# Performance work log

Hardware: AMD Instinct MI355X
Metric: run time of the kernel (lower is better)

## Reference

```python
import jax, jax.numpy as jnp
import numpy as np
import math

H = 2048          # hidden_size
NH = 16           # num_attn_heads
HD = H // NH      # attn head dim = 128
NFW = 4           # num_lact_heads
FD = H // NFW     # fw head dim = 512
DH = FD           # inter_multi = 1.0
CHUNK = 512       # lact_chunk_size
WINDOW = 2048     # window_size
ROPE_BASE = 500000.0
BASE_LR_INV = math.log(math.expm1(0.001))  # inv_softplus(1e-3)


def rmsnorm(x, w, eps=1e-6):
    return x * jax.lax.rsqrt(jnp.mean(x * x, axis=-1, keepdims=True) + eps) * w


def l2norm(x, eps=1e-12):
    return x * jax.lax.rsqrt(jnp.sum(x * x, axis=-1, keepdims=True) + eps)


def rope(x):  # x: [b, h, s, d], half-split convention
    d = x.shape[-1]
    s = x.shape[2]
    inv = 1.0 / (ROPE_BASE ** (jnp.arange(d // 2, dtype=jnp.float32) / (d // 2)))
    f = jnp.arange(s, dtype=jnp.float32)[:, None] * inv[None, :]  # [s, d/2]
    cos, sin = jnp.cos(f), jnp.sin(f)
    x1, x2 = x[..., : d // 2], x[..., d // 2:]
    return jnp.concatenate([x1 * cos - x2 * sin, x2 * cos + x1 * sin], axis=-1)


def setup_inputs() -> dict:
    key = jax.random.key(0)
    ks = jax.random.split(key, 8)
    b, s = 2, 2048
    return {
        "hidden_states": jax.random.normal(ks[0], (b, s, H), jnp.float32),
        "qkv_w": jax.random.normal(ks[1], (3 * H, H), jnp.float32) / math.sqrt(H),
        "q_norm_w": jnp.ones((H,), jnp.float32),
        "k_norm_w": jnp.ones((H,), jnp.float32),
        "qk_scale": jnp.ones((H, 2), jnp.float32),
        "qk_offset": jnp.zeros((H, 2), jnp.float32),
        "lr_w": jax.random.normal(ks[2], (3 * NFW, H), jnp.float32) / math.sqrt(H),
        "lr_b": jnp.zeros((3 * NFW,), jnp.float32),
        "w0": jax.random.normal(ks[3], (NFW, DH, FD), jnp.float32) / math.sqrt(FD),
        "w1": jax.random.normal(ks[4], (NFW, FD, DH), jnp.float32) / math.sqrt(DH),
        "w2": jax.random.normal(ks[5], (NFW, DH, FD), jnp.float32) / math.sqrt(FD),
        "ttt_norm_w": jnp.ones((FD,), jnp.float32),
        "o_proj_w": jax.random.normal(ks[6], (H, H), jnp.float32) / math.sqrt(H),
    }


def reference(hidden_states, qkv_w, q_norm_w, k_norm_w, qk_scale, qk_offset,
              lr_w, lr_b, w0, w1, w2, ttt_norm_w, o_proj_w):
    x = hidden_states
    b, s, _ = x.shape
    nc = s // CHUNK

    qkv = x @ qkv_w.T
    q, k, v = jnp.split(qkv, 3, axis=-1)
    q = rmsnorm(q, q_norm_w)
    k = rmsnorm(k, k_norm_w)

    # ---- TTT (fast-weight SwiGLU) branch ----
    fq = jax.nn.silu(q * qk_scale[:, 0] + qk_offset[:, 0])
    fk = jax.nn.silu(k * qk_scale[:, 1] + qk_offset[:, 1])
    fv = jax.nn.silu(v)
    tohead = lambda t: t.reshape(b, s, NFW, FD).transpose(0, 2, 1, 3)  # [b,h,s,d]
    fq, fk, fv = l2norm(tohead(fq)), l2norm(tohead(fk)), tohead(fv)

    lr = jax.nn.softplus(x @ lr_w.T + lr_b + BASE_LR_INV)          # [b,s,3*NFW]
    lr = lr.reshape(b, s, 3, NFW).transpose(2, 0, 3, 1)[..., None]  # [3,b,h,s,1]
    lr0, lr1, lr2 = lr[0], lr[1], lr[2]

    chunkify = lambda t: t.reshape(b, NFW, nc, CHUNK, -1).transpose(2, 0, 1, 3, 4)
    qs, ks_, vs = chunkify(fq), chunkify(fk), chunkify(fv)
    l0s, l1s, l2s = chunkify(lr0), chunkify(lr1), chunkify(lr2)

    w0b = jnp.broadcast_to(w0, (b,) + w0.shape)
    w1b = jnp.broadcast_to(w1, (b,) + w1.shape)
    w2b = jnp.broadcast_to(w2, (b,) + w2.shape)

    def step(carry, xs):
        w0c, w1c, w2c = carry
        qc, kc, vc, l0, l1, l2 = xs
        # apply current fast weights to queries (strictly causal across chunks)
        hq = jax.nn.silu(jnp.einsum('bhcd,bhed->bhce', qc, w0c)) * \
             jnp.einsum('bhcd,bhed->bhce', qc, w2c)
        oc = jnp.einsum('bhce,bhde->bhcd', hq, w1c)
        # gradient-descent update on dot-product loss -sum(v * f(k))
        g1 = jnp.einsum('bhcd,bhed->bhce', kc, w0c)
        g2 = jnp.einsum('bhcd,bhed->bhce', kc, w2c)
        gate = jax.nn.silu(g1)
        hidden = gate * g2
        dhidden = jnp.einsum('bhcd,bhde->bhce', vc, w1c)  # w1^T v
        dh2 = dhidden * gate
        sig = jax.nn.sigmoid(g1)
        dh1 = dhidden * g2 * (sig * (1.0 + g1 * (1.0 - sig)))  # silu'(g1)
        w1n = w1c + jnp.einsum('bhcd,bhce->bhde', l1 * vc, hidden)
        w0n = w0c + jnp.einsum('bhce,bhcd->bhed', l0 * dh1, kc)
        w2n = w2c + jnp.einsum('bhce,bhcd->bhed', l2 * dh2, kc)
        return (w0n, w1n, w2n), oc

    _, o_chunks = jax.lax.scan(step, (w0b, w1b, w2b), (qs, ks_, vs, l0s, l1s, l2s))
    o_ttt = o_chunks.transpose(1, 2, 0, 3, 4).reshape(b, NFW, s, FD)
    o_ttt = rmsnorm(o_ttt, ttt_norm_w)
    o_ttt = o_ttt.transpose(0, 2, 1, 3).reshape(b, s, H)

    # ---- sliding-window attention branch ----
    qa = rope(q.reshape(b, s, NH, HD).transpose(0, 2, 1, 3))
    ka = rope(k.reshape(b, s, NH, HD).transpose(0, 2, 1, 3))
    va = v.reshape(b, s, NH, HD).transpose(0, 2, 1, 3)
    scores = jnp.einsum('bhqd,bhkd->bhqk', qa, ka) / math.sqrt(HD)
    i = jnp.arange(s)
    mask = (i[:, None] >= i[None, :]) & (i[:, None] - i[None, :] < WINDOW)
    scores = jnp.where(mask, scores, jnp.float32(-1e9))
    p = jax.nn.softmax(scores, axis=-1)
    attn = jnp.einsum('bhqk,bhkd->bhqd', p, va).transpose(0, 2, 1, 3).reshape(b, s, H)

    return (attn + o_ttt) @ o_proj_w.T
```

## Files before the change

kernel.cpp:

```cpp
#include <hip/hip_runtime.h>
#include <hip/hip_bf16.h>
#include <math.h>

using bf16 = __hip_bfloat16;

namespace {

constexpr int cH = 2048;
constexpr int cNH = 16;
constexpr int cHD = 128;
constexpr int cNFW = 4;
constexpr int cFD = 512;
constexpr int cS = 2048;
constexpr float cRSQRT_HD = 0.08838834764831845f;
constexpr long ZL_ = 262144;
constexpr long ZG_ = 1048576;

typedef __attribute__((ext_vector_type(8))) short short8;
typedef __attribute__((ext_vector_type(4))) float f32x4;

__device__ __forceinline__ float sigmoidf_(float x) { return 1.0f / (1.0f + __expf(-x)); }
__device__ __forceinline__ float b2f(bf16 v) { return __bfloat162float(v); }
__device__ __forceinline__ bf16 f2b(float v) { return __float2bfloat16(v); }
__device__ __forceinline__ unsigned short f2bu(float f) {
  return __builtin_bit_cast(unsigned short, __float2bfloat16(f));
}

#if defined(__has_builtin)
#if __has_builtin(__builtin_amdgcn_global_load_lds)
#define HAVE_GLOAD 1
#endif
#endif

__device__ __forceinline__ void gload16(const bf16* g, short* ldsbase) {
#ifdef HAVE_GLOAD
  __builtin_amdgcn_global_load_lds((const __attribute__((address_space(1))) void*)g,
                                   (__attribute__((address_space(3))) void*)ldsbase, 16, 0, 0);
#else
  const int l = threadIdx.x & 63;
  *(uint4*)(ldsbase + l * 8) = *(const uint4*)g;
#endif
}

__device__ __forceinline__ void stage16(const bf16* src, short* dst) {
  *(uint4*)dst = *(const uint4*)src;
  *(uint4*)(dst + 8) = *(const uint4*)(src + 8);
}

__device__ __forceinline__ void store1(float* p, float v) { *p = v; }
__device__ __forceinline__ void store1(bf16* p, float v) { *p = f2b(v); }

template <int AMODE, int BMODE>
__device__ __forceinline__ void mm_core(const bf16* __restrict__ Ab, int lda,
                                        const bf16* __restrict__ Bb, int ldb, int K,
                                        const float* __restrict__ sc,
                                        short* As, short* Bs, f32x4 acc[4][4]) {
  const int t = threadIdx.x, lane = t & 63, g = lane >> 4, c16 = lane & 15;
  const int wv = t >> 6, wm = (wv >> 1) * 64, wn = (wv & 1) * 64;
  for (int k0 = 0; k0 < K; k0 += 32) {
    __syncthreads();
    if constexpr (AMODE == 0) {
      const int ch = wv * 2;
      const bf16* g0 = Ab + (size_t)(ch * 16 + (lane >> 2)) * lda + k0 + (lane & 3) * 8;
      gload16(g0, &As[ch * 512]);
      gload16(g0 + (size_t)16 * lda, &As[ch * 512 + 512]);
    } else {
      const int kk = t >> 3, mseg = (t & 7) * 16;
      const float s = sc[k0 + kk];
      const bf16* p = Ab + (size_t)(k0 + kk) * lda + mseg;
#pragma unroll
      for (int i = 0; i < 16; ++i) As[(mseg + i) * 32 + kk] = (short)f2bu(b2f(p[i]) * s);
    }
    if constexpr (BMODE == 0) {
      const int ch = wv * 2;
      const bf16* g0 = Bb + (size_t)(ch * 16 + (lane >> 2)) * ldb + k0 + (lane & 3) * 8;
      gload16(g0, &Bs[ch * 512]);
      gload16(g0 + (size_t)16 * ldb, &Bs[ch * 512 + 512]);
    } else {
      const int kk = t >> 3, cseg = (t & 7) * 16;
      const short* p = (const short*)(Bb + (size_t)(k0 + kk) * ldb + cseg);
#pragma unroll
      for (int i = 0; i < 16; ++i) Bs[(cseg + i) * 32 + kk] = p[i];
    }
    __syncthreads();
    short8 af[4], bfr[4];
#pragma unroll
    for (int mi = 0; mi < 4; ++mi) af[mi] = *(const short8*)&As[(wm + mi * 16 + c16) * 32 + g * 8];
#pragma unroll
    for (int ni = 0; ni < 4; ++ni) bfr[ni] = *(const short8*)&Bs[(wn + ni * 16 + c16) * 32 + g * 8];
#pragma unroll
    for (int mi = 0; mi < 4; ++mi)
#pragma unroll
      for (int ni = 0; ni < 4; ++ni)
        acc[mi][ni] = __builtin_amdgcn_mfma_f32_16x16x32_bf16(af[mi], bfr[ni], acc[mi][ni], 0, 0, 0);
  }
}

template <bool ACC, bool MIR, typename TC>
__device__ __forceinline__ void mm_store(TC* Cb, bf16* Mb, int ldc, int rb, int cb, f32x4 acc[4][4]) {
  const int t = threadIdx.x, lane = t & 63, g = lane >> 4, c16 = lane & 15;
  const int wv = t >> 6, wm = (wv >> 1) * 64, wn = (wv & 1) * 64;
  const int rbase = rb + wm, cbase = cb + wn;
#pragma unroll
  for (int mi = 0; mi < 4; ++mi)
#pragma unroll
    for (int ni = 0; ni < 4; ++ni) {
      const int col = cbase + ni * 16 + c16;
#pragma unroll
      for (int r = 0; r < 4; ++r) {
        const int row = rbase + mi * 16 + g * 4 + r;
        TC* cp = Cb + (size_t)row * ldc + col;
        if constexpr (ACC) {
          float nv = *cp + acc[mi][ni][r];
          *cp = nv;
          if constexpr (MIR) Mb[(size_t)row * ldc + col] = f2b(nv);
        } else {
          store1(cp, acc[mi][ni][r]);
        }
      }
    }
}

template <typename TC, int BMODE>
__global__ __launch_bounds__(256) void k_mm(const bf16* __restrict__ A, int lda, long zsa,
                                            const bf16* __restrict__ B, int ldb, long zsb,
                                            TC* __restrict__ C, int ldc, long zsc, int K) {
  __shared__ short As[128 * 32];
  __shared__ short Bs[128 * 32];
  const int z = blockIdx.z;
  const bf16* Ab = A + (size_t)z * zsa + (size_t)blockIdx.y * 128 * lda;
  const bf16* Bb = (BMODE == 0) ? (B + (size_t)z * zsb + (size_t)blockIdx.x * 128 * ldb)
                                : (B + (size_t)z * zsb + blockIdx.x * 128);
  f32x4 acc[4][4];
  const f32x4 zero4 = {0.f, 0.f, 0.f, 0.f};
#pragma unroll
  for (int i = 0; i < 4; ++i)
#pragma unroll
    for (int j = 0; j < 4; ++j) acc[i][j] = zero4;
  mm_core<0, BMODE>(Ab, lda, Bb, ldb, K, nullptr, As, Bs, acc);
  mm_store<false, false>(C + (size_t)z * zsc, (bf16*)nullptr, ldc, blockIdx.y * 128, blockIdx.x * 128, acc);
}

__global__ __launch_bounds__(256) void k_fuse1(const bf16* __restrict__ fq, const bf16* __restrict__ fk,
                                               const bf16* __restrict__ fv,
                                               const bf16* __restrict__ w0b, const bf16* __restrict__ w1bc,
                                               const bf16* __restrict__ w2b,
                                               bf16* __restrict__ hq, bf16* __restrict__ trH,
                                               bf16* __restrict__ trD1, bf16* __restrict__ trD2,
                                               bf16* __restrict__ trK, bf16* __restrict__ trV,
                                               const float* __restrict__ lr0, const float* __restrict__ lr1,
                                               const float* __restrict__ lr2,
                                               const bf16* __restrict__ occPrev,
                                               const float* __restrict__ tw, bf16* __restrict__ y,
                                               int chunk) {
  __shared__ short S[12800];
  __shared__ float red[4];
  const int id = blockIdx.x, t = threadIdx.x;
  const size_t choff = (size_t)chunk * 262144;

  if (id < 512) {
    const int bh = id >> 6, tile = id & 63, by = tile >> 3, bx = tile & 7;
    const int lane = t & 63, g = lane >> 4, c16 = lane & 15, wv = t >> 6;
    const int wm = (wv >> 1) * 32, wn = (wv & 1) * 32;
    const bf16* Aq = fq + (size_t)bh * ZG_ + choff + (size_t)(by * 64) * cFD;
    const bf16* Ak = fk + (size_t)bh * ZG_ + choff + (size_t)(by * 64) * cFD;
    const bf16* Av = fv + (size_t)bh * ZG_ + choff + (size_t)(by * 64) * cFD;
    const bf16* B0 = w0b + (size_t)bh * ZL_ + (size_t)(bx * 64) * cFD;
    const bf16* B2 = w2b + (size_t)bh * ZL_ + (size_t)(bx * 64) * cFD;
    const bf16* B1 = w1bc + (size_t)bh * ZL_ + bx * 64;

    f32x4 acc[5][2][2];
    const f32x4 zero4 = {0.f, 0.f, 0.f, 0.f};
#pragma unroll
    for (int v = 0; v < 5; ++v)
#pragma unroll
      for (int i = 0; i < 2; ++i)
#pragma unroll
        for (int j = 0; j < 2; ++j) acc[v][i][j] = zero4;

    const int srow = wv * 16 + (lane >> 2), scol = (lane & 3) * 8;
    for (int k0 = 0; k0 < 512; k0 += 32) {
      __syncthreads();
      gload16(Aq + (size_t)srow * cFD + k0 + scol, &S[0 + wv * 512]);
      gload16(Ak + (size_t)srow * cFD + k0 + scol, &S[2048 + wv * 512]);
      gload16(Av + (size_t)srow * cFD + k0 + scol, &S[4096 + wv * 512]);
      gload16(B0 + (size_t)srow * cFD + k0 + scol, &S[6144 + wv * 512]);
      gload16(B2 + (size_t)srow * cFD + k0 + scol, &S[8192 + wv * 512]);
      {
        const int e = t & 63, kg = t >> 6;
        unsigned short u[8] __attribute__((aligned(16)));
#pragma unroll
        for (int i = 0; i < 8; ++i)
          u[i] = *(const unsigned short*)(B1 + (size_t)(k0 + kg * 8 + i) * cFD + e);
        *(uint4*)&S[10240 + e * 40 + kg * 8] = *(uint4*)u;
      }
      __syncthreads();
      short8 aq[2], ak[2], av[2], b0[2], b2[2], b1[2];
#pragma unroll
      for (int mi = 0; mi < 2; ++mi) {
        const int ro = (wm + mi * 16 + c16) * 32 + g * 8;
        aq[mi] = *(const short8*)&S[0 + ro];
        ak[mi] = *(const short8*)&S[2048 + ro];
        av[mi] = *(const short8*)&S[4096 + ro];
      }
#pragma unroll
      for (int ni = 0; ni < 2; ++ni) {
        const int ro = (wn + ni * 16 + c16) * 32 + g * 8;
        b0[ni] = *(const short8*)&S[6144 + ro];
        b2[ni] = *(const short8*)&S[8192 + ro];
        b1[ni] = *(const short8*)&S[10240 + (wn + ni * 16 + c16) * 40 + g * 8];
      }
#pragma unroll
      for (int mi = 0; mi < 2; ++mi)
#pragma unroll
        for (int ni = 0; ni < 2; ++ni) {
          acc[0][mi][ni] = __builtin_amdgcn_mfma_f32_16x16x32_bf16(aq[mi], b0[ni], acc[0][mi][ni], 0, 0, 0);
          acc[1][mi][ni] = __builtin_amdgcn_mfma_f32_16x16x32_bf16(aq[mi], b2[ni], acc[1][mi][ni], 0, 0, 0);
          acc[2][mi][ni] = __builtin_amdgcn_mfma_f32_16x16x32_bf16(ak[mi], b0[ni], acc[2][mi][ni], 0, 0, 0);
          acc[3][mi][ni] = __builtin_amdgcn_mfma_f32_16x16x32_bf16(ak[mi], b2[ni], acc[3][mi][ni], 0, 0, 0);
          acc[4][mi][ni] = __builtin_amdgcn_mfma_f32_16x16x32_bf16(av[mi], b1[ni], acc[4][mi][ni], 0, 0, 0);
        }
    }

    float l0v[2][4], l2v[2][4];
#pragma unroll
    for (int mi = 0; mi < 2; ++mi)
#pragma unroll
      for (int r = 0; r < 4; ++r) {
        const int row = by * 64 + wm + mi * 16 + g * 4 + r;
        l0v[mi][r] = lr0[bh * 2048 + chunk * 512 + row];
        l2v[mi][r] = lr2[bh * 2048 + chunk * 512 + row];
      }
#pragma unroll
    for (int mi = 0; mi < 2; ++mi)
#pragma unroll
      for (int ni = 0; ni < 2; ++ni)
#pragma unroll
        for (int r = 0; r < 4; ++r) {
          float hq1 = acc[0][mi][ni][r], hq2 = acc[1][mi][ni][r];
          float g1 = acc[2][mi][ni][r], g2 = acc[3][mi][ni][r], dh = acc[4][mi][ni][r];
          acc[0][mi][ni][r] = hq1 * sigmoidf_(hq1) * hq2;
          float sg = sigmoidf_(g1);
          float gate = g1 * sg;
          acc[1][mi][ni][r] = gate * g2;
          acc[2][mi][ni][r] = l0v[mi][r] * dh * g2 * (sg * (1.0f + g1 * (1.0f - sg)));
          acc[3][mi][ni][r] = l2v[mi][r] * dh * gate;
        }

    short* Ts = S;
    bf16* dst0 = hq + (size_t)bh * ZL_;
    bf16* dstT[3] = {trH + (size_t)bh * ZL_, trD1 + (size_t)bh * ZL_, trD2 + (size_t)bh * ZL_};
#pragma unroll
    for (int rd = 0; rd < 4; ++rd) {
      __syncthreads();
#pragma unroll
      for (int mi = 0; mi < 2; ++mi)
#pragma unroll
        for (int ni = 0; ni < 2; ++ni)
#pragma unroll
          for (int r = 0; r < 4; ++r) {
            const int row = wm + mi * 16 + g * 4 + r, col = wn + ni * 16 + c16;
            if (rd == 0) Ts[row * 66 + col] = (short)f2bu(acc[0][mi][ni][r]);
            else Ts[col * 66 + row] = (short)f2bu(acc[rd][mi][ni][r]);
          }
      __syncthreads();
      const int rr = t >> 2, cs = (t & 3) * 16;
      unsigned short u[16] __attribute__((aligned(16)));
#pragma unroll
      for (int i = 0; i < 16; ++i) u[i] = (unsigned short)Ts[rr * 66 + cs + i];
      bf16* dp = (rd == 0) ? (dst0 + (size_t)(by * 64 + rr) * cFD + bx * 64 + cs)
                           : (dstT[rd - 1] + (size_t)(bx * 64 + rr) * cFD + by * 64 + cs);
      *(uint4*)dp = *(uint4*)u;
      *(uint4*)(dp + 8) = *(uint4*)(u + 8);
    }
  } else if (id < 1536) {
    short* Ts = S;
    const int id2 = id - 512;
    const int var = id2 >> 9, bh = (id2 >> 6) & 7, by = (id2 >> 3) & 7, bx = id2 & 7;
    const bf16* src = ((var == 0) ? fk : fv) + choff + (size_t)bh * ZG_;
    bf16* dst = ((var == 0) ? trK : trV) + (size_t)bh * ZL_;
    {
      const int rr = t >> 2, cseg = (t & 3) * 16;
      if (var == 0) {
        stage16(src + (size_t)(by * 64 + rr) * cFD + bx * 64 + cseg, &Ts[rr * 72 + cseg]);
      } else {
        const float s = lr1[bh * 2048 + chunk * 512 + by * 64 + rr];
        const bf16* p = src + (size_t)(by * 64 + rr) * cFD + bx * 64 + cseg;
        unsigned short u[16] __attribute__((aligned(16)));
#pragma unroll
        for (int i = 0; i < 16; ++i) u[i] = f2bu(b2f(p[i]) * s);
        *(uint4*)&Ts[rr * 72 + cseg] = *(uint4*)u;
        *(uint4*)&Ts[rr * 72 + cseg + 8] = *(uint4*)(u + 8);
      }
    }
    __syncthreads();
    {
      const int oc_ = t >> 2, rseg = (t & 3) * 16;
      unsigned short u[16] __attribute__((aligned(16)));
#pragma unroll
      for (int i = 0; i < 16; ++i) u[i] = (unsigned short)Ts[(rseg + i) * 72 + oc_];
      bf16* dp = dst + (size_t)(bx * 64 + oc_) * cFD + by * 64 + rseg;
      *(uint4*)dp = *(uint4*)u;
      *(uint4*)(dp + 8) = *(uint4*)(u + 8);
    }
  } else {
    const int rrow = id - 1536;
    const int bh = rrow >> 9, rr = rrow & 511;
    const bf16* src = occPrev + ((size_t)bh * 512 + rr) * 512;
    float v0 = b2f(src[t]), v1 = b2f(src[t + 256]);
    float ss = v0 * v0 + v1 * v1;
    for (int d = 32; d; d >>= 1) ss += __shfl_down(ss, d);
    if ((t & 63) == 0) red[t >> 6] = ss;
    __syncthreads();
    const float rstd = rsqrtf((red[0] + red[1] + red[2] + red[3]) / cFD + 1e-6f);
    const int si = (chunk - 1) * 512 + rr;
    bf16* dst = y + ((size_t)((bh >> 2) * cS) + si) * cH + (bh & 3) * cFD;
    dst[t] = f2b(b2f(dst[t]) + v0 * rstd * tw[t]);
    dst[t + 256] = f2b(b2f(dst[t + 256]) + v1 * rstd * tw[t + 256]);
  }
}

__global__ __launch_bounds__(256) void k_updna(const bf16* __restrict__ trV, const bf16* __restrict__ trH,
                                               const bf16* __restrict__ trD1, const bf16* __restrict__ trD2,
                                               const bf16* __restrict__ trK,
                                               const bf16* __restrict__ hq, const bf16* __restrict__ w1bc,
                                               float* w0s, float* w1s, float* w2s,
                                               bf16* w0b, bf16* w1bn, bf16* w2b,
                                               bf16* __restrict__ occCur) {
  __shared__ short Sh[8192];
  const int id = blockIdx.x, t = threadIdx.x;
  if (id < 384) {
    short* As = Sh;
    short* Bs = Sh + 4096;
    const int z = id >> 4, tile = id & 15, by = tile >> 2, bx = tile & 3;
    const int var = z >> 3, bh = z & 7;
    const bf16 *Aa, *Bb;
    float* W;
    bf16* M;
    if (var == 0) {
      Aa = trV + (size_t)bh * ZL_ + (size_t)by * 128 * cFD;
      Bb = trH + (size_t)bh * ZL_ + (size_t)bx * 128 * cFD;
      W = w1s + (size_t)bh * ZL_; M = w1bn + (size_t)bh * ZL_;
    } else if (var == 1) {
      Aa = trD1 + (size_t)bh * ZL_ + (size_t)by * 128 * cFD;
      Bb = trK + (size_t)bh * ZL_ + (size_t)bx * 128 * cFD;
      W = w0s + (size_t)bh * ZL_; M = w0b + (size_t)bh * ZL_;
    } else {
      Aa = trD2 + (size_t)bh * ZL_ + (size_t)by * 128 * cFD;
      Bb = trK + (size_t)bh * ZL_ + (size_t)bx * 128 * cFD;
      W = w2s + (size_t)bh * ZL_; M = w2b + (size_t)bh * ZL_;
    }
    f32x4 acc[4][4];
    const f32x4 zero4 = {0.f, 0.f, 0.f, 0.f};
#pragma unroll
    for (int i = 0; i < 4; ++i)
#pragma unroll
      for (int j = 0; j < 4; ++j) acc[i][j] = zero4;
    mm_core<0, 0>(Aa, cFD, Bb, cFD, cFD, nullptr, As, Bs, acc);
    mm_store<true, true>(W, M, cFD, by * 128, bx * 128, acc);
  } else {
    const int id2 = id - 384;
    const int bh = id2 >> 6, tile = id2 & 63, by = tile >> 3, bx = tile & 7;
    const int lane = t & 63, g = lane >> 4, c16 = lane & 15, wv = t >> 6;
    const int wm = (wv >> 1) * 32, wn = (wv & 1) * 32;
    const bf16* Aa = hq + (size_t)bh * ZL_ + (size_t)(by * 64) * cFD;
    const bf16* Bb = w1bc + (size_t)bh * ZL_ + (size_t)(bx * 64) * cFD;
    short* As = Sh;
    short* Bs = Sh + 2048;
    f32x4 acc[2][2];
    const f32x4 zero4 = {0.f, 0.f, 0.f, 0.f};
#pragma unroll
    for (int i = 0; i < 2; ++i)
#pragma unroll
      for (int j = 0; j < 2; ++j) acc[i][j] = zero4;
    for (int k0 = 0; k0 < 512; k0 += 32) {
      __syncthreads();
      {
        const int srow = wv * 16 + (lane >> 2), scol = (lane & 3) * 8;
        gload16(Aa + (size_t)srow * cFD + k0 + scol, &As[wv * 512]);
        gload16(Bb + (size_t)srow * cFD + k0 + scol, &Bs[wv * 512]);
      }
      __syncthreads();
      short8 af[2], bfr[2];
#pragma unroll
      for (int mi = 0; mi < 2; ++mi) af[mi] = *(const short8*)&As[(wm + mi * 16 + c16) * 32 + g * 8];
#pragma unroll
      for (int ni = 0; ni < 2; ++ni) bfr[ni] = *(const short8*)&Bs[(wn + ni * 16 + c16) * 32 + g * 8];
#pragma unroll
      for (int mi = 0; mi < 2; ++mi)
#pragma unroll
        for (int ni = 0; ni < 2; ++ni)
          acc[mi][ni] = __builtin_amdgcn_mfma_f32_16x16x32_bf16(af[mi], bfr[ni], acc[mi][ni], 0, 0, 0);
    }
    bf16* C = occCur + (size_t)bh * ZL_;
#pragma unroll
    for (int mi = 0; mi < 2; ++mi)
#pragma unroll
      for (int ni = 0; ni < 2; ++ni) {
        const int col = bx * 64 + wn + ni * 16 + c16;
#pragma unroll
        for (int r = 0; r < 4; ++r) {
          const int row = by * 64 + wm + mi * 16 + g * 4 + r;
          C[(size_t)row * cFD + col] = f2b(acc[mi][ni][r]);
        }
      }
  }
}

__global__ __launch_bounds__(256) void k_normcvt(const bf16* __restrict__ occ,
                                                 const float* __restrict__ tw, bf16* __restrict__ y,
                                                 const float* __restrict__ opw, bf16* __restrict__ opwb,
                                                 int chunk) {
  __shared__ float red[4];
  const int id = blockIdx.x, t = threadIdx.x;
  if (id < 4096) {
    const int bh = id >> 9, rr = id & 511;
    const bf16* src = occ + ((size_t)bh * 512 + rr) * 512;
    float v0 = b2f(src[t]), v1 = b2f(src[t + 256]);
    float ss = v0 * v0 + v1 * v1;
    for (int d = 32; d; d >>= 1) ss += __shfl_down(ss, d);
    if ((t & 63) == 0) red[t >> 6] = ss;
    __syncthreads();
    const float rstd = rsqrtf((red[0] + red[1] + red[2] + red[3]) / cFD + 1e-6f);
    const int si = chunk * 512 + rr;
    bf16* dst = y + ((size_t)((bh >> 2) * cS) + si) * cH + (bh & 3) * cFD;
    dst[t] = f2b(b2f(dst[t]) + v0 * rstd * tw[t]);
    dst[t + 256] = f2b(b2f(dst[t + 256]) + v1 * rstd * tw[t + 256]);
  } else {
    const size_t i = ((size_t)(id - 4096) * 256 + t) * 8;
    float4 a = *(const float4*)(opw + i), b = *(const float4*)(opw + i + 4);
    unsigned short u[8] __attribute__((aligned(16)));
    u[0] = f2bu(a.x); u[1] = f2bu(a.y); u[2] = f2bu(a.z); u[3] = f2bu(a.w);
    u[4] = f2bu(b.x); u[5] = f2bu(b.y); u[6] = f2bu(b.z); u[7] = f2bu(b.w);
    *(uint4*)(opwb + i) = *(uint4*)u;
  }
}

__global__ __launch_bounds__(256) void k_cvt(const float* __restrict__ src, bf16* __restrict__ dst) {
  const size_t i = ((size_t)blockIdx.x * 256 + threadIdx.x) * 8;
  float4 a = *(const float4*)(src + i), b = *(const float4*)(src + i + 4);
  unsigned short u[8] __attribute__((aligned(16)));
  u[0] = f2bu(a.x); u[1] = f2bu(a.y); u[2] = f2bu(a.z); u[3] = f2bu(a.w);
  u[4] = f2bu(b.x); u[5] = f2bu(b.y); u[6] = f2bu(b.z); u[7] = f2bu(b.w);
  *(uint4*)(dst + i) = *(uint4*)u;
}

__global__ __launch_bounds__(256) void k_prep(const float* __restrict__ x, const float* __restrict__ qkv_w,
                                              const float* __restrict__ w0, const float* __restrict__ w1,
                                              const float* __restrict__ w2,
                                              const float* __restrict__ lr_w, const float* __restrict__ lr_b,
                                              bf16* __restrict__ xb, bf16* __restrict__ qkvwb,
                                              float* __restrict__ w0s, float* __restrict__ w1s,
                                              float* __restrict__ w2s,
                                              float* __restrict__ ct, float* __restrict__ stb,
                                              float* lr0, float* lr1, float* lr2, float base) {
  const int id = blockIdx.x, t = threadIdx.x;
  if (id < 4096) {
    const size_t i = ((size_t)id * 256 + t) * 8;
    float4 a = *(const float4*)(x + i), b = *(const float4*)(x + i + 4);
    unsigned short u[8] __attribute__((aligned(16)));
    u[0] = f2bu(a.x); u[1] = f2bu(a.y); u[2] = f2bu(a.z); u[3] = f2bu(a.w);
    u[4] = f2bu(b.x); u[5] = f2bu(b.y); u[6] = f2bu(b.z); u[7] = f2bu(b.w);
    *(uint4*)(xb + i) = *(uint4*)u;
  } else if (id < 10240) {
    const size_t i = ((size_t)(id - 4096) * 256 + t) * 8;
    float4 a = *(const float4*)(qkv_w + i), b = *(const float4*)(qkv_w + i + 4);
    unsigned short u[8] __attribute__((aligned(16)));
    u[0] = f2bu(a.x); u[1] = f2bu(a.y); u[2] = f2bu(a.z); u[3] = f2bu(a.w);
    u[4] = f2bu(b.x); u[5] = f2bu(b.y); u[6] = f2bu(b.z); u[7] = f2bu(b.w);
    *(uint4*)(qkvwb + i) = *(uint4*)u;
  } else if (id < 16384) {
    const int sub = id - 10240;
    const int w = sub >> 11, blk = sub & 2047;
    const size_t i = ((size_t)blk * 256 + t) * 4;
    const int f = (int)((i >> 18) & 3);
    const size_t off = i & 262143;
    const float* src = (w == 0) ? w0 : (w == 1) ? w1 : w2;
    float* dst = (w == 0) ? w0s : (w == 1) ? w1s : w2s;
    *(float4*)(dst + i) = *(const float4*)(src + (size_t)f * 262144 + off);
  } else if (id < 16896) {
    const int gid = (id - 16384) * 256 + t;
    const int si = gid >> 6, jj = gid & 63;
    float inv = powf(500000.0f, -(float)jj / 64.0f);
    float ang = (float)si * inv;
    ct[(size_t)si * 64 + jj] = cosf(ang);
    stb[(size_t)si * 64 + jj] = sinf(ang);
  } else {
    const int token = id - 16896, b_ = token >> 11, si = token & 2047;
    const int wv = t >> 6, lane = t & 63;
    const float* xr = x + (size_t)token * cH;
#pragma unroll
    for (int jj = 0; jj < 3; ++jj) {
      const int j = wv * 3 + jj;
      const float* wr = lr_w + (size_t)j * cH;
      float s = 0.f;
      for (int k = lane; k < cH; k += 64) s += xr[k] * wr[k];
      for (int d = 32; d; d >>= 1) s += __shfl_down(s, d);
      if (lane == 0) {
        float v = s + lr_b[j] + base;
        float sp = (v > 15.f) ? v : log1pf(expf(v));
        const int tt = j >> 2, f = j & 3;
        float* dst = (tt == 0 ? lr0 : tt == 1 ? lr1 : lr2);
        dst[(size_t)(b_ * cNFW + f) * cS + si] = sp;
      }
    }
  }
}

__global__ __launch_bounds__(256) void k_normrope(bf16* __restrict__ qkvh,
                                                  const float* __restrict__ qnw, const float* __restrict__ knw,
                                                  const float* __restrict__ ct, const float* __restrict__ stb,
                                                  bf16* __restrict__ qa, bf16* __restrict__ ka) {
  const int token = blockIdx.x, b_ = token >> 11, si = token & 2047;
  const int t = threadIdx.x;
  __shared__ float buf[cH];
  __shared__ float red[4];
  bf16* base = qkvh + (size_t)token * 3 * cH;
  for (int pass = 0; pass < 2; ++pass) {
    __syncthreads();
    bf16* src = base + pass * cH;
    const float* nw = pass ? knw : qnw;
    float ss = 0.f;
    for (int i = t; i < cH; i += 256) {
      float v = b2f(src[i]);
      buf[i] = v;
      ss += v * v;
    }
    for (int d = 32; d; d >>= 1) ss += __shfl_down(ss, d);
    if ((t & 63) == 0) red[t >> 6] = ss;
    __syncthreads();
    const float rstd = rsqrtf((red[0] + red[1] + red[2] + red[3]) / cH + 1e-6f);
    for (int i = t; i < cH; i += 256) {
      float v = buf[i] * rstd * nw[i];
      buf[i] = v;
      src[i] = f2b(v);
    }
    __syncthreads();
    bf16* dst = pass ? ka : qa;
    const float scale = pass ? 1.f : cRSQRT_HD;
    const int hh = t >> 4, j0 = (t & 15) * 4;
    const float* cr = ct + (size_t)si * 64 + j0;
    const float* sr = stb + (size_t)si * 64 + j0;
    bf16* drow = dst + ((size_t)(b_ * cNH + hh) * cS + si) * cHD;
    unsigned short u1[4] __attribute__((aligned(8))), u2[4] __attribute__((aligned(8)));
#pragma unroll
    for (int i = 0; i < 4; ++i) {
      float x1 = buf[hh * cHD + j0 + i], x2 = buf[hh * cHD + 64 + j0 + i];
      u1[i] = f2bu((x1 * cr[i] - x2 * sr[i]) * scale);
      u2[i] = f2bu((x2 * cr[i] + x1 * sr[i]) * scale);
    }
    *(uint2*)(drow + j0) = *(uint2*)u1;
    *(uint2*)(drow + 64 + j0) = *(uint2*)u2;
  }
}

__global__ __launch_bounds__(256) void k_vtr(const bf16* __restrict__ qkvh, bf16* __restrict__ vt) {
  const int tile = blockIdx.x, h = blockIdx.y, b_ = blockIdx.z;
  __shared__ short Ts[64 * 136];
  const int t = threadIdx.x;
  {
    const int r = t >> 2, seg = (t & 3) * 32;
    const bf16* src = qkvh + ((size_t)(b_ * cS) + tile * 64 + r) * 3 * cH + 2 * cH + h * cHD + seg;
    stage16(src, &Ts[r * 136 + seg]);
    stage16(src + 16, &Ts[r * 136 + seg + 16]);
  }
  __syncthreads();
  {
    const int d = t >> 1, seg2 = (t & 1) * 32;
    unsigned short u[32] __attribute__((aligned(16)));
#pragma unroll
    for (int i = 0; i < 32; ++i) u[i] = (unsigned short)Ts[(seg2 + i) * 136 + d];
    bf16* dp = vt + ((size_t)(b_ * cNH + h) * cHD + d) * cS + tile * 64 + seg2;
    *(uint4*)dp = *(uint4*)u;
    *(uint4*)(dp + 8) = *(uint4*)(u + 8);
    *(uint4*)(dp + 16) = *(uint4*)(u + 16);
    *(uint4*)(dp + 24) = *(uint4*)(u + 24);
  }
}

__global__ __launch_bounds__(256) void k_fqkv(const bf16* __restrict__ qkvh,
                                              const float* __restrict__ qk_scale,
                                              const float* __restrict__ qk_offset,
                                              bf16* fq, bf16* fk, bf16* fv) {
  const int token = blockIdx.x, b_ = token >> 11, si = token & 2047;
  const int t = threadIdx.x;
  const bf16* base = qkvh + (size_t)token * 3 * cH;
#pragma unroll
  for (int pass = 0; pass < 2; ++pass) {
    const bf16* src = base + pass * cH;
    bf16* fdst = pass ? fk : fq;
    const int head = t >> 6, lane = t & 63;
    float f[8];
    float ss2 = 0.f;
#pragma unroll
    for (int k = 0; k < 8; ++k) {
      const int idx = head * cFD + lane + k * 64;
      float v = b2f(src[idx]);
      float u = v * qk_scale[idx * 2 + pass] + qk_offset[idx * 2 + pass];
      float fv_ = u * sigmoidf_(u);
      f[k] = fv_;
      ss2 += fv_ * fv_;
    }
    for (int d = 1; d < 64; d <<= 1) ss2 += __shfl_xor(ss2, d);
    const float sc2 = rsqrtf(ss2 + 1e-12f);
    bf16* dst = fdst + ((size_t)(b_ * cNFW + head) * cS + si) * cFD;
#pragma unroll
    for (int k = 0; k < 8; ++k) dst[lane + k * 64] = f2b(f[k] * sc2);
  }
  const bf16* vr = base + 2 * cH;
  for (int i = t; i < cH; i += 256) {
    float v = b2f(vr[i]);
    fv[((size_t)(b_ * cNFW + (i >> 9)) * cS + si) * cFD + (i & 511)] = f2b(v * sigmoidf_(v));
  }
}

__global__ __launch_bounds__(512) void k_attn6(const bf16* __restrict__ qa, const bf16* __restrict__ ka,
                                               const bf16* __restrict__ vt, bf16* __restrict__ y) {
  const int id = blockIdx.x;
  const int xcd = id & 7;
  const int j = id >> 3;
  const int p = j & 7;
  const int hb = (j >> 3) * 8 + xcd;
  const int h = hb & 15, b_ = hb >> 4;
  __shared__ short KsP[9216];
  __shared__ short Vts[128 * 72];
  const int t = threadIdx.x, lane = t & 63, g = lane >> 4, c16 = lane & 15, wv = t >> 6;
  const size_t hbq = (size_t)(b_ * cNH + h) * cS;
  const bf16* vb = vt + (size_t)(b_ * cNH + h) * (size_t)(cHD * cS);
  const int r = t >> 3, seg = (t & 7) * 16;
  const int dv = t >> 2, seg2 = (t & 3) * 16;
  const f32x4 zero4 = {0.f, 0.f, 0.f, 0.f};

  for (int half = 0; half < 2; ++half) {
    const int qt = half ? p : 15 - p;
    const int q0 = qt * 128;
    const int nkt = 2 * qt + 2;
    short8 qf[4];
    {
      const bf16* qsrc = qa + (hbq + q0 + wv * 16 + c16) * cHD;
#pragma unroll
      for (int ks = 0; ks < 4; ++ks) qf[ks] = *(const short8*)(qsrc + ks * 32 + g * 8);
    }
    f32x4 o[8];
#pragma unroll
    for (int i = 0; i < 8; ++i) o[i] = zero4;
    float m[4], l[4];
#pragma unroll
    for (int rr = 0; rr < 4; ++rr) { m[rr] = -1e30f; l[rr] = 0.f; }

    uint4 kp0, kp1, vp0, vp1;
    {
      const bf16* ksrc = ka + (hbq + r) * cHD + seg;
      kp0 = *(const uint4*)ksrc; kp1 = *(const uint4*)(ksrc + 8);
      const bf16* vsrc = vb + (size_t)dv * cS + seg2;
      vp0 = *(const uint4*)vsrc; vp1 = *(const uint4*)(vsrc + 8);
    }

    for (int kt = 0; kt < nkt; ++kt) {
      __syncthreads();
      {
        short* kd = &KsP[r * 136 + seg];
        *(uint4*)kd = kp0; *(uint4*)(kd + 8) = kp1;
        short* vd = &Vts[dv * 72 + seg2];
        *(uint4*)vd = vp0; *(uint4*)(vd + 8) = vp1;
      }
      __syncthreads();
      if (kt + 1 < nkt) {
        const bf16* ksrc = ka + (hbq + (kt + 1) * 64 + r) * cHD + seg;
        kp0 = *(const uint4*)ksrc; kp1 = *(const uint4*)(ksrc + 8);
        const bf16* vsrc = vb + (size_t)dv * cS + (kt + 1) * 64 + seg2;
        vp0 = *(const uint4*)vsrc; vp1 = *(const uint4*)(vsrc + 8);
      } else if (half == 0) {
        const bf16* ksrc = ka + (hbq + r) * cHD + seg;
        kp0 = *(const uint4*)ksrc; kp1 = *(const uint4*)(ksrc + 8);
        const bf16* vsrc = vb + (size_t)dv * cS + seg2;
        vp0 = *(const uint4*)vsrc; vp1 = *(const uint4*)(vsrc + 8);
      }

      f32x4 s4[4];
#pragma unroll
      for (int ni = 0; ni < 4; ++ni) s4[ni] = zero4;
      __builtin_amdgcn_s_setprio(1);
#pragma unroll
      for (int ks = 0; ks < 4; ++ks) {
#pragma unroll
        for (int ni = 0; ni < 4; ++ni) {
          short8 bb = *(const short8*)&KsP[(ni * 16 + c16) * 136 + ks * 32 + g * 8];
          s4[ni] = __builtin_amdgcn_mfma_f32_16x16x32_bf16(qf[ks], bb, s4[ni], 0, 0, 0);
        }
      }
      __builtin_amdgcn_s_setprio(0);
      __syncthreads();
      if (kt * 64 + 64 > q0) {
#pragma unroll
        for (int ni = 0; ni < 4; ++ni) {
          const int kv = kt * 64 + ni * 16 + c16;
#pragma unroll
          for (int rr = 0; rr < 4; ++rr) {
            const int qr = q0 + wv * 16 + g * 4 + rr;
            if (kv > qr) s4[ni][rr] = -1e9f;
          }
        }
      }
      float mx[4];
#pragma unroll
      for (int rr = 0; rr < 4; ++rr)
        mx[rr] = fmaxf(fmaxf(s4[0][rr], s4[1][rr]), fmaxf(s4[2][rr], s4[3][rr]));
#pragma unroll
      for (int d = 1; d < 16; d <<= 1)
#pragma unroll
        for (int rr = 0; rr < 4; ++rr) mx[rr] = fmaxf(mx[rr], __shfl_xor(mx[rr], d));
      bool need = false;
#pragma unroll
      for (int rr = 0; rr < 4; ++rr) need |= (mx[rr] > m[rr] + 8.f);
      if (__any(need)) {
        float corr[4];
#pragma unroll
        for (int rr = 0; rr < 4; ++rr) {
          float mn = fmaxf(m[rr], mx[rr]);
          corr[rr] = __expf(m[rr] - mn);
          m[rr] = mn;
        }
#pragma unroll
        for (int rr = 0; rr < 4; ++rr) l[rr] *= corr[rr];
#pragma unroll
        for (int nf = 0; nf < 8; ++nf)
#pragma unroll
          for (int rr = 0; rr < 4; ++rr) o[nf][rr] *= corr[rr];
      }
      float psum[4] = {0.f, 0.f, 0.f, 0.f};
#pragma unroll
      for (int ni = 0; ni < 4; ++ni)
#pragma unroll
        for (int rr = 0; rr < 4; ++rr) {
          float pp = __expf(s4[ni][rr] - m[rr]);
          s4[ni][rr] = pp;
          psum[rr] += pp;
        }
#pragma unroll
      for (int d = 1; d < 16; d <<= 1)
#pragma unroll
        for (int rr = 0; rr < 4; ++rr) psum[rr] += __shfl_xor(psum[rr], d);
#pragma unroll
      for (int rr = 0; rr < 4; ++rr) l[rr] += psum[rr];
      short* pw = &KsP[wv * 1152];
#pragma unroll
      for (int ni = 0; ni < 4; ++ni)
#pragma unroll
        for (int rr = 0; rr < 4; ++rr)
          pw[(g * 4 + rr) * 72 + ni * 16 + c16] = (short)f2bu(s4[ni][rr]);
      __builtin_amdgcn_s_setprio(1);
#pragma unroll
      for (int ks2 = 0; ks2 < 2; ++ks2) {
        short8 a = *(const short8*)&pw[c16 * 72 + ks2 * 32 + g * 8];
#pragma unroll
        for (int nf = 0; nf < 8; ++nf) {
          short8 bb = *(const short8*)&Vts[(nf * 16 + c16) * 72 + ks2 * 32 + g * 8];
          o[nf] = __builtin_amdgcn_mfma_f32_16x16x32_bf16(a, bb, o[nf], 0, 0, 0);
        }
      }
      __builtin_amdgcn_s_setprio(0);
    }
    float inv[4];
#pragma unroll
    for (int rr = 0; rr < 4; ++rr) inv[rr] = 1.f / l[rr];
#pragma unroll
    for (int nf = 0; nf < 8; ++nf)
#pragma unroll
      for (int rr = 0; rr < 4; ++rr) {
        const size_t row = (size_t)(b_ * cS) + q0 + wv * 16 + g * 4 + rr;
        y[row * cH + h * cHD + nf * 16 + c16] = f2b(o[nf][rr] * inv[rr]);
      }
  }
}

}

extern "C" void kernel_launch(void* const* d_in, const int* in_sizes, int n_in,
                              void* d_out, int out_size, void* d_ws, size_t ws_size,
                              hipStream_t stream) {
  (void)in_sizes; (void)n_in; (void)out_size; (void)ws_size;
  const float* x         = (const float*)d_in[0];
  const float* qkv_w     = (const float*)d_in[1];
  const float* q_norm_w  = (const float*)d_in[2];
  const float* k_norm_w  = (const float*)d_in[3];
  const float* qk_scale  = (const float*)d_in[4];
  const float* qk_offset = (const float*)d_in[5];
  const float* lr_w      = (const float*)d_in[6];
  const float* lr_b      = (const float*)d_in[7];
  const float* w0        = (const float*)d_in[8];
  const float* w1        = (const float*)d_in[9];
  const float* w2        = (const float*)d_in[10];
  const float* ttt_nw    = (const float*)d_in[11];
  const float* o_proj_w  = (const float*)d_in[12];
  float* out = (float*)d_out;

  char* Wb = (char*)d_ws;
  bf16* qkvh = (bf16*)Wb;
  bf16* hq   = (bf16*)(Wb + 0UL);
  bf16* trH  = (bf16*)(Wb + 4194304UL);
  bf16* trD1 = (bf16*)(Wb + 8388608UL);
  bf16* trD2 = (bf16*)(Wb + 12582912UL);
  bf16* trK  = (bf16*)(Wb + 16777216UL);
  bf16* trV  = (bf16*)(Wb + 20971520UL);
  bf16* occA = (bf16*)(Wb + 25165824UL);
  bf16* occB = (bf16*)(Wb + 29360128UL);
  bf16* w0b  = (bf16*)(Wb + 33554432UL);
  bf16* w1b0 = (bf16*)(Wb + 37748736UL);
  bf16* w2b  = (bf16*)(Wb + 41943040UL);
  bf16* w1b1 = (bf16*)(Wb + 46137344UL);
  bf16* opwb = (bf16*)(Wb + 0UL);
  size_t off = 50331648UL;
  bf16* fqb = (bf16*)(Wb + off); off += 16777216UL;
  bf16* fkb = (bf16*)(Wb + off); off += 16777216UL;
  bf16* fvb = (bf16*)(Wb + off); off += 16777216UL;
  float* w0s = (float*)(Wb + off); off += 8388608UL;
  float* w1s = (float*)(Wb + off); off += 8388608UL;
  float* w2s = (float*)(Wb + off); off += 8388608UL;
  float* lr0 = (float*)(Wb + off); off += 65536UL;
  float* lr1 = (float*)(Wb + off); off += 65536UL;
  float* lr2 = (float*)(Wb + off); off += 65536UL;
  bf16* y = (bf16*)(Wb + off); off += 16777216UL;
  float* ct  = (float*)(Wb + off); off += 524288UL;
  float* stb = (float*)(Wb + off); off += 524288UL;
  bf16* xb = fqb;
  bf16* qkvwb = fkb;
  bf16* qa = fqb;
  bf16* ka = fkb;
  bf16* vt = fvb;
  bf16* w1m[2] = {w1b0, w1b1};
  bf16* occb[2] = {occA, occB};

  const float base_lr_inv = logf(expm1f(0.001f));
  dim3 blk(256);

  k_prep<<<dim3(20992), blk, 0, stream>>>(x, qkv_w, w0, w1, w2, lr_w, lr_b,
                                          xb, qkvwb, w0s, w1s, w2s, ct, stb,
                                          lr0, lr1, lr2, base_lr_inv);
  k_mm<bf16, 0><<<dim3(48, 32, 1), blk, 0, stream>>>(xb, 2048, 0, qkvwb, 2048, 0, qkvh, 6144, 0, 2048);
  k_normrope<<<dim3(4096), blk, 0, stream>>>(qkvh, q_norm_w, k_norm_w, ct, stb, qa, ka);
  k_vtr<<<dim3(32, 16, 2), blk, 0, stream>>>(qkvh, vt);
  k_attn6<<<dim3(256), dim3(512), 0, stream>>>(qa, ka, vt, y);
  k_fqkv<<<dim3(4096), blk, 0, stream>>>(qkvh, qk_scale, qk_offset, fqb, fkb, fvb);
  k_cvt<<<dim3(3072), blk, 0, stream>>>(w0s, w0b);

  for (int c = 0; c < 4; ++c) {
    const int g1 = (c == 0) ? 1536 : 5632;
    k_fuse1<<<dim3(g1), blk, 0, stream>>>(fqb, fkb, fvb, w0b, w1m[c & 1], w2b,
                                          hq, trH, trD1, trD2, trK, trV,
                                          lr0, lr1, lr2,
                                          (c == 0) ? occb[0] : occb[(c - 1) & 1],
                                          ttt_nw, y, c);
    k_updna<<<dim3(896), blk, 0, stream>>>(trV, trH, trD1, trD2, trK, hq, w1m[c & 1],
                                           w0s, w1s, w2s, w0b, w1m[(c + 1) & 1], w2b,
                                           occb[c & 1]);
  }
  k_normcvt<<<dim3(6144), blk, 0, stream>>>(occb[1], ttt_nw, y, o_proj_w, opwb, 3);
  k_mm<float, 0><<<dim3(16, 32, 1), blk, 0, stream>>>(y, 2048, 0, opwb, 2048, 0, out, 2048, 0, 2048);
}
```

Baseline: 726.3 us.

## Fuse post-QKV kernels, keep transposed w1 copy, enlarge GEMM K-tile and occ tiles

Merges normrope and v-transpose into one kernel, and merges the fq/fk/fv feature map, w0 conversion and a new w1 transpose into another, which cuts the launch count. k_updna now writes a transposed bf16 copy of w1 through LDS so k_fuse1 can load it with direct global-to-LDS copies instead of strided scalar gathers. The big projection GEMMs use a K-tile of 64 instead of 32, the occ GEMM uses 128x128 tiles through the shared mm_core, and the double-buffered occ arrays become one buffer. The cost is extra transpose work and LDS traffic inside k_updna, plus a larger LDS footprint in k_mm that may lower occupancy.

```diff
diff --git a/kernel.cpp b/kernel.cpp
--- a/kernel.cpp
+++ b/kernel.cpp
@@ -25,6 +25,7 @@
 __device__ __forceinline__ unsigned short f2bu(float f) {
   return __builtin_bit_cast(unsigned short, __float2bfloat16(f));
 }
+__device__ __forceinline__ float bu2f(unsigned u) { return __uint_as_float(u << 16); }
 
 #if defined(__has_builtin)
 #if __has_builtin(__builtin_amdgcn_global_load_lds)
@@ -50,49 +51,59 @@
 __device__ __forceinline__ void store1(float* p, float v) { *p = v; }
 __device__ __forceinline__ void store1(bf16* p, float v) { *p = f2b(v); }
 
-template <int AMODE, int BMODE>
+template <int BK>
 __device__ __forceinline__ void mm_core(const bf16* __restrict__ Ab, int lda,
                                         const bf16* __restrict__ Bb, int ldb, int K,
-                                        const float* __restrict__ sc,
                                         short* As, short* Bs, f32x4 acc[4][4]) {
   const int t = threadIdx.x, lane = t & 63, g = lane >> 4, c16 = lane & 15;
   const int wv = t >> 6, wm = (wv >> 1) * 64, wn = (wv & 1) * 64;
-  for (int k0 = 0; k0 < K; k0 += 32) {
+  for (int k0 = 0; k0 < K; k0 += BK) {
     __syncthreads();
-    if constexpr (AMODE == 0) {
+    if constexpr (BK == 32) {
       const int ch = wv * 2;
-      const bf16* g0 = Ab + (size_t)(ch * 16 + (lane >> 2)) * lda + k0 + (lane & 3) * 8;
-      gload16(g0, &As[ch * 512]);
-      gload16(g0 + (size_t)16 * lda, &As[ch * 512 + 512]);
+      const bf16* ga = Ab + (size_t)(ch * 16 + (lane >> 2)) * lda + k0 + (lane & 3) * 8;
+      gload16(ga, &As[ch * 512]);
+      gload16(ga + (size_t)16 * lda, &As[ch * 512 + 512]);
+      const bf16* gb = Bb + (size_t)(ch * 16 + (lane >> 2)) * ldb + k0 + (lane & 3) * 8;
+      gload16(gb, &Bs[ch * 512]);
+      gload16(gb + (size_t)16 * ldb, &Bs[ch * 512 + 512]);
     } else {
-      const int kk = t >> 3, mseg = (t & 7) * 16;
-      const float s = sc[k0 + kk];
-      const bf16* p = Ab + (size_t)(k0 + kk) * lda + mseg;
-#pragma unroll
-      for (int i = 0; i < 16; ++i) As[(mseg + i) * 32 + kk] = (short)f2bu(b2f(p[i]) * s);
-    }
-    if constexpr (BMODE == 0) {
-      const int ch = wv * 2;
-      const bf16* g0 = Bb + (size_t)(ch * 16 + (lane >> 2)) * ldb + k0 + (lane & 3) * 8;
-      gload16(g0, &Bs[ch * 512]);
-      gload16(g0 + (size_t)16 * ldb, &Bs[ch * 512 + 512]);
+#pragma unroll
+      for (int i = 0; i < 4; ++i) {
+        const int rbase = wv * 32 + i * 8;
+        gload16(Ab + (size_t)(rbase + (lane >> 3)) * lda + k0 + (lane & 7) * 8, &As[rbase * 64]);
+        gload16(Bb + (size_t)(rbase + (lane >> 3)) * ldb + k0 + (lane & 7) * 8, &Bs[rbase * 64]);
+      }
+    }
+    __syncthreads();
+    if constexpr (BK == 32) {
+      short8 af[4], bfr[4];
+#pragma unroll
+      for (int mi = 0; mi < 4; ++mi) af[mi] = *(const short8*)&As[(wm + mi * 16 + c16) * 32 + g * 8];
+#pragma unroll
+      for (int ni = 0; ni < 4; ++ni) bfr[ni] = *(const short8*)&Bs[(wn + ni * 16 + c16) * 32 + g * 8];
+#pragma unroll
+      for (int mi = 0; mi < 4; ++mi)
+#pragma unroll
+        for (int ni = 0; ni < 4; ++ni)
+          acc[mi][ni] = __builtin_amdgcn_mfma_f32_16x16x32_bf16(af[mi], bfr[ni], acc[mi][ni], 0, 0, 0);
     } else {
-      const int kk = t >> 3, cseg = (t & 7) * 16;
-      const short* p = (const short*)(Bb + (size_t)(k0 + kk) * ldb + cseg);
-#pragma unroll
-      for (int i = 0; i < 16; ++i) Bs[(cseg + i) * 32 + kk] = p[i];
-    }
-    __syncthreads();
-    short8 af[4], bfr[4];
-#pragma unroll
-    for (int mi = 0; mi < 4; ++mi) af[mi] = *(const short8*)&As[(wm + mi * 16 + c16) * 32 + g * 8];
-#pragma unroll
-    for (int ni = 0; ni < 4; ++ni) bfr[ni] = *(const short8*)&Bs[(wn + ni * 16 + c16) * 32 + g * 8];
-#pragma unroll
-    for (int mi = 0; mi < 4; ++mi)
-#pragma unroll
-      for (int ni = 0; ni < 4; ++ni)
-        acc[mi][ni] = __builtin_amdgcn_mfma_f32_16x16x32_bf16(af[mi], bfr[ni], acc[mi][ni], 0, 0, 0);
+#pragma unroll
+      for (int ks = 0; ks < 2; ++ks) {
+        short8 af[4], bfr[4];
+#pragma unroll
+        for (int mi = 0; mi < 4; ++mi)
+          af[mi] = *(const short8*)&As[(wm + mi * 16 + c16) * 64 + ks * 32 + g * 8];
+#pragma unroll
+        for (int ni = 0; ni < 4; ++ni)
+          bfr[ni] = *(const short8*)&Bs[(wn + ni * 16 + c16) * 64 + ks * 32 + g * 8];
+#pragma unroll
+        for (int mi = 0; mi < 4; ++mi)
+#pragma unroll
+          for (int ni = 0; ni < 4; ++ni)
+            acc[mi][ni] = __builtin_amdgcn_mfma_f32_16x16x32_bf16(af[mi], bfr[ni], acc[mi][ni], 0, 0, 0);
+      }
+    }
   }
 }
 
@@ -121,39 +132,37 @@
     }
 }
 
-template <typename TC, int BMODE>
-__global__ __launch_bounds__(256) void k_mm(const bf16* __restrict__ A, int lda, long zsa,
-                                            const bf16* __restrict__ B, int ldb, long zsb,
-                                            TC* __restrict__ C, int ldc, long zsc, int K) {
-  __shared__ short As[128 * 32];
-  __shared__ short Bs[128 * 32];
-  const int z = blockIdx.z;
-  const bf16* Ab = A + (size_t)z * zsa + (size_t)blockIdx.y * 128 * lda;
-  const bf16* Bb = (BMODE == 0) ? (B + (size_t)z * zsb + (size_t)blockIdx.x * 128 * ldb)
-                                : (B + (size_t)z * zsb + blockIdx.x * 128);
+template <typename TC>
+__global__ __launch_bounds__(256) void k_mm(const bf16* __restrict__ A, int lda,
+                                            const bf16* __restrict__ B, int ldb,
+                                            TC* __restrict__ C, int ldc, int K) {
+  __shared__ short As[128 * 64];
+  __shared__ short Bs[128 * 64];
+  const bf16* Ab = A + (size_t)blockIdx.y * 128 * lda;
+  const bf16* Bb = B + (size_t)blockIdx.x * 128 * ldb;
   f32x4 acc[4][4];
   const f32x4 zero4 = {0.f, 0.f, 0.f, 0.f};
 #pragma unroll
   for (int i = 0; i < 4; ++i)
 #pragma unroll
     for (int j = 0; j < 4; ++j) acc[i][j] = zero4;
-  mm_core<0, BMODE>(Ab, lda, Bb, ldb, K, nullptr, As, Bs, acc);
-  mm_store<false, false>(C + (size_t)z * zsc, (bf16*)nullptr, ldc, blockIdx.y * 128, blockIdx.x * 128, acc);
+  mm_core<64>(Ab, lda, Bb, ldb, K, As, Bs, acc);
+  mm_store<false, false>(C, (bf16*)nullptr, ldc, blockIdx.y * 128, blockIdx.x * 128, acc);
 }
 
 __global__ __launch_bounds__(256) void k_fuse1(const bf16* __restrict__ fq, const bf16* __restrict__ fk,
                                                const bf16* __restrict__ fv,
-                                               const bf16* __restrict__ w0b, const bf16* __restrict__ w1bc,
+                                               const bf16* __restrict__ w0b, const bf16* __restrict__ w1t,
                                                const bf16* __restrict__ w2b,
                                                bf16* __restrict__ hq, bf16* __restrict__ trH,
                                                bf16* __restrict__ trD1, bf16* __restrict__ trD2,
                                                bf16* __restrict__ trK, bf16* __restrict__ trV,
                                                const float* __restrict__ lr0, const float* __restrict__ lr1,
                                                const float* __restrict__ lr2,
-                                               const bf16* __restrict__ occPrev,
+                                               const bf16* __restrict__ occ,
                                                const float* __restrict__ tw, bf16* __restrict__ y,
                                                int chunk) {
-  __shared__ short S[12800];
+  __shared__ short S[12288];
   __shared__ float red[4];
   const int id = blockIdx.x, t = threadIdx.x;
   const size_t choff = (size_t)chunk * 262144;
@@ -167,7 +176,7 @@
     const bf16* Av = fv + (size_t)bh * ZG_ + choff + (size_t)(by * 64) * cFD;
     const bf16* B0 = w0b + (size_t)bh * ZL_ + (size_t)(bx * 64) * cFD;
     const bf16* B2 = w2b + (size_t)bh * ZL_ + (size_t)(bx * 64) * cFD;
-    const bf16* B1 = w1bc + (size_t)bh * ZL_ + bx * 64;
+    const bf16* B1 = w1t + (size_t)bh * ZL_ + (size_t)(bx * 64) * cFD;
 
     f32x4 acc[5][2][2];
     const f32x4 zero4 = {0.f, 0.f, 0.f, 0.f};
@@ -186,14 +195,7 @@
       gload16(Av + (size_t)srow * cFD + k0 + scol, &S[4096 + wv * 512]);
       gload16(B0 + (size_t)srow * cFD + k0 + scol, &S[6144 + wv * 512]);
       gload16(B2 + (size_t)srow * cFD + k0 + scol, &S[8192 + wv * 512]);
-      {
-        const int e = t & 63, kg = t >> 6;
-        unsigned short u[8] __attribute__((aligned(16)));
-#pragma unroll
-        for (int i = 0; i < 8; ++i)
-          u[i] = *(const unsigned short*)(B1 + (size_t)(k0 + kg * 8 + i) * cFD + e);
-        *(uint4*)&S[10240 + e * 40 + kg * 8] = *(uint4*)u;
-      }
+      gload16(B1 + (size_t)srow * cFD + k0 + scol, &S[10240 + wv * 512]);
       __syncthreads();
       short8 aq[2], ak[2], av[2], b0[2], b2[2], b1[2];
 #pragma unroll
@@ -208,7 +210,7 @@
         const int ro = (wn + ni * 16 + c16) * 32 + g * 8;
         b0[ni] = *(const short8*)&S[6144 + ro];
         b2[ni] = *(const short8*)&S[8192 + ro];
-        b1[ni] = *(const short8*)&S[10240 + (wn + ni * 16 + c16) * 40 + g * 8];
+        b1[ni] = *(const short8*)&S[10240 + ro];
       }
 #pragma unroll
       for (int mi = 0; mi < 2; ++mi)
@@ -306,7 +308,7 @@
   } else {
     const int rrow = id - 1536;
     const int bh = rrow >> 9, rr = rrow & 511;
-    const bf16* src = occPrev + ((size_t)bh * 512 + rr) * 512;
+    const bf16* src = occ + ((size_t)bh * 512 + rr) * 512;
     float v0 = b2f(src[t]), v1 = b2f(src[t + 256]);
     float ss = v0 * v0 + v1 * v1;
     for (int d = 32; d; d >>= 1) ss += __shfl_down(ss, d);
@@ -325,30 +327,26 @@
                                                const bf16* __restrict__ trK,
                                                const bf16* __restrict__ hq, const bf16* __restrict__ w1bc,
                                                float* w0s, float* w1s, float* w2s,
-                                               bf16* w0b, bf16* w1bn, bf16* w2b,
-                                               bf16* __restrict__ occCur) {
-  __shared__ short Sh[8192];
+                                               bf16* w0b, bf16* w1bn, bf16* w2b, bf16* w1t,
+                                               bf16* __restrict__ occ) {
+  __shared__ short Sh[8704];
   const int id = blockIdx.x, t = threadIdx.x;
+  const int lane = t & 63, g = lane >> 4, c16 = lane & 15, wv = t >> 6;
   if (id < 384) {
     short* As = Sh;
     short* Bs = Sh + 4096;
     const int z = id >> 4, tile = id & 15, by = tile >> 2, bx = tile & 3;
     const int var = z >> 3, bh = z & 7;
     const bf16 *Aa, *Bb;
-    float* W;
-    bf16* M;
     if (var == 0) {
       Aa = trV + (size_t)bh * ZL_ + (size_t)by * 128 * cFD;
       Bb = trH + (size_t)bh * ZL_ + (size_t)bx * 128 * cFD;
-      W = w1s + (size_t)bh * ZL_; M = w1bn + (size_t)bh * ZL_;
     } else if (var == 1) {
       Aa = trD1 + (size_t)bh * ZL_ + (size_t)by * 128 * cFD;
       Bb = trK + (size_t)bh * ZL_ + (size_t)bx * 128 * cFD;
-      W = w0s + (size_t)bh * ZL_; M = w0b + (size_t)bh * ZL_;
     } else {
       Aa = trD2 + (size_t)bh * ZL_ + (size_t)by * 128 * cFD;
       Bb = trK + (size_t)bh * ZL_ + (size_t)bx * 128 * cFD;
-      W = w2s + (size_t)bh * ZL_; M = w2b + (size_t)bh * ZL_;
     }
     f32x4 acc[4][4];
     const f32x4 zero4 = {0.f, 0.f, 0.f, 0.f};
@@ -356,54 +354,73 @@
     for (int i = 0; i < 4; ++i)
 #pragma unroll
       for (int j = 0; j < 4; ++j) acc[i][j] = zero4;
-    mm_core<0, 0>(Aa, cFD, Bb, cFD, cFD, nullptr, As, Bs, acc);
-    mm_store<true, true>(W, M, cFD, by * 128, bx * 128, acc);
+    mm_core<32>(Aa, cFD, Bb, cFD, cFD, As, Bs, acc);
+    if (var == 1) {
+      mm_store<true, true>(w0s + (size_t)bh * ZL_, w0b + (size_t)bh * ZL_, cFD, by * 128, bx * 128, acc);
+    } else if (var == 2) {
+      mm_store<true, true>(w2s + (size_t)bh * ZL_, w2b + (size_t)bh * ZL_, cFD, by * 128, bx * 128, acc);
+    } else {
+      float* W = w1s + (size_t)bh * ZL_;
+      bf16* M = w1bn + (size_t)bh * ZL_;
+      const int wm = (wv >> 1) * 64, wn = (wv & 1) * 64;
+#pragma unroll
+      for (int mi = 0; mi < 4; ++mi)
+#pragma unroll
+        for (int ni = 0; ni < 4; ++ni) {
+          const int col = bx * 128 + wn + ni * 16 + c16;
+#pragma unroll
+          for (int r = 0; r < 4; ++r) {
+            const int row = by * 128 + wm + mi * 16 + g * 4 + r;
+            float nv = W[(size_t)row * cFD + col] + acc[mi][ni][r];
+            W[(size_t)row * cFD + col] = nv;
+            M[(size_t)row * cFD + col] = f2b(nv);
+            acc[mi][ni][r] = nv;
+          }
+        }
+      bf16* T = w1t + (size_t)bh * ZL_;
+      short* Ts = Sh;
+#pragma unroll
+      for (int rd = 0; rd < 2; ++rd) {
+        __syncthreads();
+        if (wn == rd * 64) {
+#pragma unroll
+          for (int mi = 0; mi < 4; ++mi)
+#pragma unroll
+            for (int ni = 0; ni < 4; ++ni) {
+              const int cc = ni * 16 + c16;
+              unsigned short u[4] __attribute__((aligned(8)));
+#pragma unroll
+              for (int r = 0; r < 4; ++r) u[r] = f2bu(acc[mi][ni][r]);
+              *(uint2*)&Ts[cc * 136 + wm + mi * 16 + g * 4] = *(uint2*)u;
+            }
+        }
+        __syncthreads();
+        const int cc = t >> 2, seg = (t & 3) * 32;
+        unsigned short u[32] __attribute__((aligned(16)));
+#pragma unroll
+        for (int i = 0; i < 32; ++i) u[i] = (unsigned short)Ts[cc * 136 + seg + i];
+        bf16* dp = T + (size_t)(bx * 128 + rd * 64 + cc) * cFD + by * 128 + seg;
+        *(uint4*)dp = *(uint4*)u;
+        *(uint4*)(dp + 8) = *(uint4*)(u + 8);
+        *(uint4*)(dp + 16) = *(uint4*)(u + 16);
+        *(uint4*)(dp + 24) = *(uint4*)(u + 24);
+      }
+    }
   } else {
+    short* As = Sh;
+    short* Bs = Sh + 4096;
     const int id2 = id - 384;
-    const int bh = id2 >> 6, tile = id2 & 63, by = tile >> 3, bx = tile & 7;
-    const int lane = t & 63, g = lane >> 4, c16 = lane & 15, wv = t >> 6;
-    const int wm = (wv >> 1) * 32, wn = (wv & 1) * 32;
-    const bf16* Aa = hq + (size_t)bh * ZL_ + (size_t)(by * 64) * cFD;
-    const bf16* Bb = w1bc + (size_t)bh * ZL_ + (size_t)(bx * 64) * cFD;
-    short* As = Sh;
-    short* Bs = Sh + 2048;
-    f32x4 acc[2][2];
+    const int bh = id2 >> 4, tile = id2 & 15, by = tile >> 2, bx = tile & 3;
+    const bf16* Aa = hq + (size_t)bh * ZL_ + (size_t)by * 128 * cFD;
+    const bf16* Bb = w1bc + (size_t)bh * ZL_ + (size_t)bx * 128 * cFD;
+    f32x4 acc[4][4];
     const f32x4 zero4 = {0.f, 0.f, 0.f, 0.f};
 #pragma unroll
-    for (int i = 0; i < 2; ++i)
-#pragma unroll
-      for (int j = 0; j < 2; ++j) acc[i][j] = zero4;
-    for (int k0 = 0; k0 < 512; k0 += 32) {
-      __syncthreads();
-      {
-        const int srow = wv * 16 + (lane >> 2), scol = (lane & 3) * 8;
-        gload16(Aa + (size_t)srow * cFD + k0 + scol, &As[wv * 512]);
-        gload16(Bb + (size_t)srow * cFD + k0 + scol, &Bs[wv * 512]);
-      }
-      __syncthreads();
-      short8 af[2], bfr[2];
-#pragma unroll
-      for (int mi = 0; mi < 2; ++mi) af[mi] = *(const short8*)&As[(wm + mi * 16 + c16) * 32 + g * 8];
-#pragma unroll
-      for (int ni = 0; ni < 2; ++ni) bfr[ni] = *(const short8*)&Bs[(wn + ni * 16 + c16) * 32 + g * 8];
-#pragma unroll
-      for (int mi = 0; mi < 2; ++mi)
-#pragma unroll
-        for (int ni = 0; ni < 2; ++ni)
-          acc[mi][ni] = __builtin_amdgcn_mfma_f32_16x16x32_bf16(af[mi], bfr[ni], acc[mi][ni], 0, 0, 0);
-    }
-    bf16* C = occCur + (size_t)bh * ZL_;
-#pragma unroll
-    for (int mi = 0; mi < 2; ++mi)
-#pragma unroll
-      for (int ni = 0; ni < 2; ++ni) {
-        const int col = bx * 64 + wn + ni * 16 + c16;
-#pragma unroll
-        for (int r = 0; r < 4; ++r) {
-          const int row = by * 64 + wm + mi * 16 + g * 4 + r;
-          C[(size_t)row * cFD + col] = f2b(acc[mi][ni][r]);
-        }
-      }
+    for (int i = 0; i < 4; ++i)
+#pragma unroll
+      for (int j = 0; j < 4; ++j) acc[i][j] = zero4;
+    mm_core<32>(Aa, cFD, Bb, cFD, cFD, As, Bs, acc);
+    mm_store<false, false>(occ + (size_t)bh * ZL_, (bf16*)nullptr, cFD, by * 128, bx * 128, acc);
   }
 }
 
@@ -434,15 +451,6 @@
     u[4] = f2bu(b.x); u[5] = f2bu(b.y); u[6] = f2bu(b.z); u[7] = f2bu(b.w);
     *(uint4*)(opwb + i) = *(uint4*)u;
   }
-}
-
-__global__ __launch_bounds__(256) void k_cvt(const float* __restrict__ src, bf16* __restrict__ dst) {
-  const size_t i = ((size_t)blockIdx.x * 256 + threadIdx.x) * 8;
-  float4 a = *(const float4*)(src + i), b = *(const float4*)(src + i + 4);
-  unsigned short u[8] __attribute__((aligned(16)));
-  u[0] = f2bu(a.x); u[1] = f2bu(a.y); u[2] = f2bu(a.z); u[3] = f2bu(a.w);
-  u[4] = f2bu(b.x); u[5] = f2bu(b.y); u[6] = f2bu(b.z); u[7] = f2bu(b.w);
-  *(uint4*)(dst + i) = *(uint4*)u;
 }
 
 __global__ __launch_bounds__(256) void k_prep(const float* __restrict__ x, const float* __restrict__ qkv_w,
@@ -507,110 +515,146 @@
   }
 }
 
-__global__ __launch_bounds__(256) void k_normrope(bf16* __restrict__ qkvh,
-                                                  const float* __restrict__ qnw, const float* __restrict__ knw,
-                                                  const float* __restrict__ ct, const float* __restrict__ stb,
-                                                  bf16* __restrict__ qa, bf16* __restrict__ ka) {
-  const int token = blockIdx.x, b_ = token >> 11, si = token & 2047;
-  const int t = threadIdx.x;
-  __shared__ float buf[cH];
+__global__ __launch_bounds__(256) void k_post2(bf16* __restrict__ qkvh,
+                                               const float* __restrict__ qnw, const float* __restrict__ knw,
+                                               const float* __restrict__ ct, const float* __restrict__ stb,
+                                               bf16* __restrict__ qa, bf16* __restrict__ ka,
+                                               bf16* __restrict__ vt) {
+  __shared__ short smem[8704];
   __shared__ float red[4];
-  bf16* base = qkvh + (size_t)token * 3 * cH;
-  for (int pass = 0; pass < 2; ++pass) {
+  const int id = blockIdx.x, t = threadIdx.x;
+  if (id < 4096) {
+    float* buf = (float*)smem;
+    const int token = id, b_ = token >> 11, si = token & 2047;
+    bf16* base = qkvh + (size_t)token * 3 * cH;
+    for (int pass = 0; pass < 2; ++pass) {
+      __syncthreads();
+      bf16* src = base + pass * cH;
+      const float* nw = pass ? knw : qnw;
+      float ss = 0.f;
+      for (int i = t; i < cH; i += 256) {
+        float v = b2f(src[i]);
+        buf[i] = v;
+        ss += v * v;
+      }
+      for (int d = 32; d; d >>= 1) ss += __shfl_down(ss, d);
+      if ((t & 63) == 0) red[t >> 6] = ss;
+      __syncthreads();
+      const float rstd = rsqrtf((red[0] + red[1] + red[2] + red[3]) / cH + 1e-6f);
+      for (int i = t; i < cH; i += 256) {
+        float v = buf[i] * rstd * nw[i];
+        buf[i] = v;
+        src[i] = f2b(v);
+      }
+      __syncthreads();
+      bf16* dst = pass ? ka : qa;
+      const float scale = pass ? 1.f : cRSQRT_HD;
+      const int hh = t >> 4, j0 = (t & 15) * 4;
+      const float* cr = ct + (size_t)si * 64 + j0;
+      const float* sr = stb + (size_t)si * 64 + j0;
+      bf16* drow = dst + ((size_t)(b_ * cNH + hh) * cS + si) * cHD;
+      unsigned short u1[4] __attribute__((aligned(8))), u2[4] __attribute__((aligned(8)));
+#pragma unroll
+      for (int i = 0; i < 4; ++i) {
+        float x1 = buf[hh * cHD + j0 + i], x2 = buf[hh * cHD + 64 + j0 + i];
+        u1[i] = f2bu((x1 * cr[i] - x2 * sr[i]) * scale);
+        u2[i] = f2bu((x2 * cr[i] + x1 * sr[i]) * scale);
+      }
+      *(uint2*)(drow + j0) = *(uint2*)u1;
+      *(uint2*)(drow + 64 + j0) = *(uint2*)u2;
+    }
+  } else {
+    short* Ts = smem;
+    const int id2 = id - 4096;
+    const int tile = id2 & 31, h = (id2 >> 5) & 15, b_ = id2 >> 9;
+    {
+      const int r = t >> 2, seg = (t & 3) * 32;
+      const bf16* src = qkvh + ((size_t)(b_ * cS) + tile * 64 + r) * 3 * cH + 2 * cH + h * cHD + seg;
+      stage16(src, &Ts[r * 136 + seg]);
+      stage16(src + 16, &Ts[r * 136 + seg + 16]);
+    }
     __syncthreads();
-    bf16* src = base + pass * cH;
-    const float* nw = pass ? knw : qnw;
-    float ss = 0.f;
+    {
+      const int d = t >> 1, seg2 = (t & 1) * 32;
+      unsigned short u[32] __attribute__((aligned(16)));
+#pragma unroll
+      for (int i = 0; i < 32; ++i) u[i] = (unsigned short)Ts[(seg2 + i) * 136 + d];
+      bf16* dp = vt + ((size_t)(b_ * cNH + h) * cHD + d) * cS + tile * 64 + seg2;
+      *(uint4*)dp = *(uint4*)u;
+      *(uint4*)(dp + 8) = *(uint4*)(u + 8);
+      *(uint4*)(dp + 16) = *(uint4*)(u + 16);
+      *(uint4*)(dp + 24) = *(uint4*)(u + 24);
+    }
+  }
+}
+
+__global__ __launch_bounds__(256) void k_mid(const bf16* __restrict__ qkvh,
+                                             const float* __restrict__ qk_scale,
+                                             const float* __restrict__ qk_offset,
+                                             bf16* fq, bf16* fk, bf16* fv,
+                                             const float* __restrict__ w0s_, bf16* __restrict__ w0b_,
+                                             const float* __restrict__ w1s_, bf16* __restrict__ w1t_) {
+  __shared__ short Ts[64 * 72];
+  const int id = blockIdx.x, t = threadIdx.x;
+  if (id < 4096) {
+    const int token = id, b_ = token >> 11, si = token & 2047;
+    const bf16* base = qkvh + (size_t)token * 3 * cH;
+#pragma unroll
+    for (int pass = 0; pass < 2; ++pass) {
+      const bf16* src = base + pass * cH;
+      bf16* fdst = pass ? fk : fq;
+      const int head = t >> 6, lane = t & 63;
+      float f[8];
+      float ss2 = 0.f;
+#pragma unroll
+      for (int k = 0; k < 8; ++k) {
+        const int idx = head * cFD + lane + k * 64;
+        float v = b2f(src[idx]);
+        float u = v * qk_scale[idx * 2 + pass] + qk_offset[idx * 2 + pass];
+        float fv_ = u * sigmoidf_(u);
+        f[k] = fv_;
+        ss2 += fv_ * fv_;
+      }
+      for (int d = 1; d < 64; d <<= 1) ss2 += __shfl_xor(ss2, d);
+      const float sc2 = rsqrtf(ss2 + 1e-12f);
+      bf16* dst = fdst + ((size_t)(b_ * cNFW + head) * cS + si) * cFD;
+#pragma unroll
+      for (int k = 0; k < 8; ++k) dst[lane + k * 64] = f2b(f[k] * sc2);
+    }
+    const bf16* vr = base + 2 * cH;
     for (int i = t; i < cH; i += 256) {
-      float v = b2f(src[i]);
-      buf[i] = v;
-      ss += v * v;
-    }
-    for (int d = 32; d; d >>= 1) ss += __shfl_down(ss, d);
-    if ((t & 63) == 0) red[t >> 6] = ss;
+      float v = b2f(vr[i]);
+      fv[((size_t)(b_ * cNFW + (i >> 9)) * cS + si) * cFD + (i & 511)] = f2b(v * sigmoidf_(v));
+    }
+  } else if (id < 7168) {
+    const size_t i = ((size_t)(id - 4096) * 256 + t) * 8;
+    float4 a = *(const float4*)(w0s_ + i), b = *(const float4*)(w0s_ + i + 4);
+    unsigned short u[8] __attribute__((aligned(16)));
+    u[0] = f2bu(a.x); u[1] = f2bu(a.y); u[2] = f2bu(a.z); u[3] = f2bu(a.w);
+    u[4] = f2bu(b.x); u[5] = f2bu(b.y); u[6] = f2bu(b.z); u[7] = f2bu(b.w);
+    *(uint4*)(w0b_ + i) = *(uint4*)u;
+  } else {
+    const int id3 = id - 7168;
+    const int bh = id3 >> 6, tile = id3 & 63, by = tile >> 3, bx = tile & 7;
+    {
+      const int rr = t >> 2, cseg = (t & 3) * 16;
+      const float* p = w1s_ + (size_t)bh * ZL_ + (size_t)(by * 64 + rr) * cFD + bx * 64 + cseg;
+      unsigned short u[16] __attribute__((aligned(16)));
+#pragma unroll
+      for (int i = 0; i < 16; ++i) u[i] = f2bu(p[i]);
+      *(uint4*)&Ts[rr * 72 + cseg] = *(uint4*)u;
+      *(uint4*)&Ts[rr * 72 + cseg + 8] = *(uint4*)(u + 8);
+    }
     __syncthreads();
-    const float rstd = rsqrtf((red[0] + red[1] + red[2] + red[3]) / cH + 1e-6f);
-    for (int i = t; i < cH; i += 256) {
-      float v = buf[i] * rstd * nw[i];
-      buf[i] = v;
-      src[i] = f2b(v);
-    }
-    __syncthreads();
-    bf16* dst = pass ? ka : qa;
-    const float scale = pass ? 1.f : cRSQRT_HD;
-    const int hh = t >> 4, j0 = (t & 15) * 4;
-    const float* cr = ct + (size_t)si * 64 + j0;
-    const float* sr = stb + (size_t)si * 64 + j0;
-    bf16* drow = dst + ((size_t)(b_ * cNH + hh) * cS + si) * cHD;
-    unsigned short u1[4] __attribute__((aligned(8))), u2[4] __attribute__((aligned(8)));
-#pragma unroll
-    for (int i = 0; i < 4; ++i) {
-      float x1 = buf[hh * cHD + j0 + i], x2 = buf[hh * cHD + 64 + j0 + i];
-      u1[i] = f2bu((x1 * cr[i] - x2 * sr[i]) * scale);
-      u2[i] = f2bu((x2 * cr[i] + x1 * sr[i]) * scale);
-    }
-    *(uint2*)(drow + j0) = *(uint2*)u1;
-    *(uint2*)(drow + 64 + j0) = *(uint2*)u2;
-  }
-}
-
-__global__ __launch_bounds__(256) void k_vtr(const bf16* __restrict__ qkvh, bf16* __restrict__ vt) {
-  const int tile = blockIdx.x, h = blockIdx.y, b_ = blockIdx.z;
-  __shared__ short Ts[64 * 136];
-  const int t = threadIdx.x;
-  {
-    const int r = t >> 2, seg = (t & 3) * 32;
-    const bf16* src = qkvh + ((size_t)(b_ * cS) + tile * 64 + r) * 3 * cH + 2 * cH + h * cHD + seg;
-    stage16(src, &Ts[r * 136 + seg]);
-    stage16(src + 16, &Ts[r * 136 + seg + 16]);
-  }
-  __syncthreads();
-  {
-    const int d = t >> 1, seg2 = (t & 1) * 32;
-    unsigned short u[32] __attribute__((aligned(16)));
-#pragma unroll
-    for (int i = 0; i < 32; ++i) u[i] = (unsigned short)Ts[(seg2 + i) * 136 + d];
-    bf16* dp = vt + ((size_t)(b_ * cNH + h) * cHD + d) * cS + tile * 64 + seg2;
-    *(uint4*)dp = *(uint4*)u;
-    *(uint4*)(dp + 8) = *(uint4*)(u + 8);
-    *(uint4*)(dp + 16) = *(uint4*)(u + 16);
-    *(uint4*)(dp + 24) = *(uint4*)(u + 24);
-  }
-}
-
-__global__ __launch_bounds__(256) void k_fqkv(const bf16* __restrict__ qkvh,
-                                              const float* __restrict__ qk_scale,
-                                              const float* __restrict__ qk_offset,
-                                              bf16* fq, bf16* fk, bf16* fv) {
-  const int token = blockIdx.x, b_ = token >> 11, si = token & 2047;
-  const int t = threadIdx.x;
-  const bf16* base = qkvh + (size_t)token * 3 * cH;
-#pragma unroll
-  for (int pass = 0; pass < 2; ++pass) {
-    const bf16* src = base + pass * cH;
-    bf16* fdst = pass ? fk : fq;
-    const int head = t >> 6, lane = t & 63;
-    float f[8];
-    float ss2 = 0.f;
-#pragma unroll
-    for (int k = 0; k < 8; ++k) {
-      const int idx = head * cFD + lane + k * 64;
-      float v = b2f(src[idx]);
-      float u = v * qk_scale[idx * 2 + pass] + qk_offset[idx * 2 + pass];
-      float fv_ = u * sigmoidf_(u);
-      f[k] = fv_;
-      ss2 += fv_ * fv_;
-    }
-    for (int d = 1; d < 64; d <<= 1) ss2 += __shfl_xor(ss2, d);
-    const float sc2 = rsqrtf(ss2 + 1e-12f);
-    bf16* dst = fdst + ((size_t)(b_ * cNFW + head) * cS + si) * cFD;
-#pragma unroll
-    for (int k = 0; k < 8; ++k) dst[lane + k * 64] = f2b(f[k] * sc2);
-  }
-  const bf16* vr = base + 2 * cH;
-  for (int i = t; i < cH; i += 256) {
-    float v = b2f(vr[i]);
-    fv[((size_t)(b_ * cNFW + (i >> 9)) * cS + si) * cFD + (i & 511)] = f2b(v * sigmoidf_(v));
+    {
+      const int oc_ = t >> 2, rseg = (t & 3) * 16;
+      unsigned short u[16] __attribute__((aligned(16)));
+#pragma unroll
+      for (int i = 0; i < 16; ++i) u[i] = (unsigned short)Ts[(rseg + i) * 72 + oc_];
+      bf16* dp = w1t_ + (size_t)bh * ZL_ + (size_t)(bx * 64 + oc_) * cFD + by * 64 + rseg;
+      *(uint4*)dp = *(uint4*)u;
+      *(uint4*)(dp + 8) = *(uint4*)(u + 8);
+    }
   }
 }
 
@@ -803,8 +847,8 @@
   bf16* trD2 = (bf16*)(Wb + 12582912UL);
   bf16* trK  = (bf16*)(Wb + 16777216UL);
   bf16* trV  = (bf16*)(Wb + 20971520UL);
-  bf16* occA = (bf16*)(Wb + 25165824UL);
-  bf16* occB = (bf16*)(Wb + 29360128UL);
+  bf16* occ  = (bf16*)(Wb + 25165824UL);
+  bf16* w1t  = (bf16*)(Wb + 29360128UL);
   bf16* w0b  = (bf16*)(Wb + 33554432UL);
   bf16* w1b0 = (bf16*)(Wb + 37748736UL);
   bf16* w2b  = (bf16*)(Wb + 41943040UL);
@@ -829,7 +873,6 @@
   bf16* ka = fkb;
   bf16* vt = fvb;
   bf16* w1m[2] = {w1b0, w1b1};
-  bf16* occb[2] = {occA, occB};
 
   const float base_lr_inv = logf(expm1f(0.001f));
   dim3 blk(256);
@@ -837,24 +880,21 @@
   k_prep<<<dim3(20992), blk, 0, stream>>>(x, qkv_w, w0, w1, w2, lr_w, lr_b,
                                           xb, qkvwb, w0s, w1s, w2s, ct, stb,
                                           lr0, lr1, lr2, base_lr_inv);
-  k_mm<bf16, 0><<<dim3(48, 32, 1), blk, 0, stream>>>(xb, 2048, 0, qkvwb, 2048, 0, qkvh, 6144, 0, 2048);
-  k_normrope<<<dim3(4096), blk, 0, stream>>>(qkvh, q_norm_w, k_norm_w, ct, stb, qa, ka);
-  k_vtr<<<dim3(32, 16, 2), blk, 0, stream>>>(qkvh, vt);
+  k_mm<bf16><<<dim3(48, 32), blk, 0, stream>>>(xb, 2048, qkvwb, 2048, qkvh, 6144, 2048);
+  k_post2<<<dim3(5120), blk, 0, stream>>>(qkvh, q_norm_w, k_norm_w, ct, stb, qa, ka, vt);
   k_attn6<<<dim3(256), dim3(512), 0, stream>>>(qa, ka, vt, y);
-  k_fqkv<<<dim3(4096), blk, 0, stream>>>(qkvh, qk_scale, qk_offset, fqb, fkb, fvb);
-  k_cvt<<<dim3(3072), blk, 0, stream>>>(w0s, w0b);
+  k_mid<<<dim3(7680), blk, 0, stream>>>(qkvh, qk_scale, qk_offset, fqb, fkb, fvb,
+                                        w0s, w0b, w1s, w1t);
 
   for (int c = 0; c < 4; ++c) {
     const int g1 = (c == 0) ? 1536 : 5632;
-    k_fuse1<<<dim3(g1), blk, 0, stream>>>(fqb, fkb, fvb, w0b, w1m[c & 1], w2b,
+    k_fuse1<<<dim3(g1), blk, 0, stream>>>(fqb, fkb, fvb, w0b, w1t, w2b,
                                           hq, trH, trD1, trD2, trK, trV,
-                                          lr0, lr1, lr2,
-                                          (c == 0) ? occb[0] : occb[(c - 1) & 1],
-                                          ttt_nw, y, c);
-    k_updna<<<dim3(896), blk, 0, stream>>>(trV, trH, trD1, trD2, trK, hq, w1m[c & 1],
-                                           w0s, w1s, w2s, w0b, w1m[(c + 1) & 1], w2b,
-                                           occb[c & 1]);
+                                          lr0, lr1, lr2, occ, ttt_nw, y, c);
+    k_updna<<<dim3(512), blk, 0, stream>>>(trV, trH, trD1, trD2, trK, hq, w1m[c & 1],
+                                           w0s, w1s, w2s, w0b, w1m[(c + 1) & 1], w2b, w1t,
+                                           occ);
   }
-  k_normcvt<<<dim3(6144), blk, 0, stream>>>(occb[1], ttt_nw, y, o_proj_w, opwb, 3);
-  k_mm<float, 0><<<dim3(16, 32, 1), blk, 0, stream>>>(y, 2048, 0, opwb, 2048, 0, out, 2048, 0, 2048);
-}
+  k_normcvt<<<dim3(6144), blk, 0, stream>>>(occ, ttt_nw, y, o_proj_w, opwb, 3);
+  k_mm<float><<<dim3(16, 32), blk, 0, stream>>>(y, 2048, opwb, 2048, out, 2048, 2048);
+}
```

Measured after the change: 714.0 us. Within noise of the previous version (-1.7%).
